# Kernel optimization log

Hardware: AMD Instinct MI355X
Metric: run time of the kernel (lower is better)

The kernel has to match this reference:

```python
import jax, jax.numpy as jnp
import numpy as np
from jax import lax

IMAGE_SIZE = 128
PATCH = 5
STRIDE = 5
ANGLES = np.deg2rad(np.arange(0, 60, 1.0))  # 60 views
N_ANGLES = len(ANGLES)


def _bilinear(img, x, y):
    # img: (H,W); x,y: arbitrary-shape sample coords; zero outside image
    H, W = img.shape
    x0 = jnp.floor(x).astype(jnp.int32)
    y0 = jnp.floor(y).astype(jnp.int32)
    x1, y1 = x0 + 1, y0 + 1
    wx = x - x0.astype(img.dtype)
    wy = y - y0.astype(img.dtype)

    def get(xi, yi):
        valid = (xi >= 0) & (xi < W) & (yi >= 0) & (yi < H)
        v = img[jnp.clip(yi, 0, H - 1), jnp.clip(xi, 0, W - 1)]
        return jnp.where(valid, v, jnp.zeros((), img.dtype))

    return (get(x0, y0) * (1 - wx) * (1 - wy) + get(x1, y0) * wx * (1 - wy)
            + get(x0, y1) * (1 - wx) * wy + get(x1, y1) * wx * wy)


def radon(img, cos_t, sin_t):
    # Discrete Radon forward projection (a=0, no FBP filter): rotate+sum line integrals.
    # img: (H,H) -> sinogram (A, H)
    H = img.shape[0]
    c = (H - 1) / 2.0
    t = jnp.arange(H, dtype=img.dtype) - c  # detector coord
    s = jnp.arange(H, dtype=img.dtype) - c  # along-ray coord
    ct = cos_t[:, None, None]
    st = sin_t[:, None, None]
    x = c + t[None, None, :] * ct - s[None, :, None] * st  # (A,S,T)
    y = c + t[None, None, :] * st + s[None, :, None] * ct
    return _bilinear(img, x, y).sum(axis=1)  # (A,T)


def _patch_starts():
    starts = []
    for i in range(0, IMAGE_SIZE, STRIDE):
        for j in range(0, IMAGE_SIZE, STRIDE):
            if i + PATCH > IMAGE_SIZE or j + PATCH > IMAGE_SIZE:
                continue
            starts.append((i, j))
    return np.array(starts, dtype=np.int32)  # (P,2)


def _build_sinogram_masks(starts):
    c = IMAGE_SIZE // 2
    P = starts.shape[0]
    masks = np.zeros((P, IMAGE_SIZE, IMAGE_SIZE), dtype=np.float32)
    for p, (i, j) in enumerate(starts):
        d0 = np.sqrt((i - c) ** 2 + (j - c) ** 2)
        d1 = np.sqrt((i + PATCH - c) ** 2 + (j + PATCH - c) ** 2)
        if d0 <= c and d1 <= c:
            masks[p, i:i + PATCH, j:j + PATCH] = 1.0
    cos_t = jnp.asarray(np.cos(ANGLES), jnp.float32)
    sin_t = jnp.asarray(np.sin(ANGLES), jnp.float32)
    # sequential map keeps memory bounded while building the 625 base sinograms
    sinos = lax.map(lambda m: radon(m, cos_t, sin_t), jnp.asarray(masks))
    return (sinos > 1e-6).astype(jnp.int32)  # (P, A, H)


def setup_inputs() -> dict:
    key = jax.random.key(0)
    ks = jax.random.split(key, 10)
    starts = _patch_starts()
    sino_masks = _build_sinogram_masks(starts)
    he = lambda k, shp, fan_in: jax.random.normal(k, shp, jnp.float32) * np.sqrt(2.0 / fan_in)
    lin_in = N_ANGLES * IMAGE_SIZE  # 7680
    return {
        "sinogram": jax.random.normal(ks[0], (N_ANGLES, IMAGE_SIZE), jnp.float32),
        "conv1_w": he(ks[1], (32, 1, 3, 3), 9),
        "conv1_b": jnp.zeros((32,), jnp.float32),
        "conv2_w": he(ks[2], (64, 32, 3, 3), 32 * 9),
        "conv2_b": jnp.zeros((64,), jnp.float32),
        "conv3_w": he(ks[3], (1, 64, 3, 3), 64 * 9),
        "conv3_b": jnp.zeros((1,), jnp.float32),
        "lin_w": he(ks[4], (PATCH * PATCH, lin_in), lin_in),
        "lin_b": jnp.zeros((PATCH * PATCH,), jnp.float32),
        "sino_masks": sino_masks,          # (625, 60, 128) int32 0/1
        "starts": jnp.asarray(starts),     # (625, 2) int32
    }


def _conv(x, w, b):
    y = lax.conv_general_dilated(x, w, (1, 1), "SAME",
                                 dimension_numbers=("NCHW", "OIHW", "NCHW"))
    return y + b[None, :, None, None]


def reference(sinogram, conv1_w, conv1_b, conv2_w, conv2_b, conv3_w, conv3_b,
              lin_w, lin_b, sino_masks, starts):
    cos_t = jnp.asarray(np.cos(ANGLES), sinogram.dtype)
    sin_t = jnp.asarray(np.sin(ANGLES), sinogram.dtype)
    # per-patch masked sinograms: (P, 1, A, S)
    masked = (sinogram[None] * sino_masks.astype(sinogram.dtype))[:, None]
    x = jax.nn.relu(_conv(masked, conv1_w, conv1_b))
    x = jax.nn.relu(_conv(x, conv2_w, conv2_b))
    x = _conv(x, conv3_w, conv3_b)
    x = x.reshape(x.shape[0], -1)                       # (P, A*S)
    patches = (x @ lin_w.T + lin_b).reshape(-1, PATCH, PATCH)
    # overlap-average reconstruction (scatter-add + count)
    rows = starts[:, 0][:, None, None] + jnp.arange(PATCH)[None, :, None]
    cols = starts[:, 1][:, None, None] + jnp.arange(PATCH)[None, None, :]
    acc = jnp.zeros((IMAGE_SIZE, IMAGE_SIZE), patches.dtype).at[rows, cols].add(patches)
    cnt = jnp.zeros((IMAGE_SIZE, IMAGE_SIZE), patches.dtype).at[rows, cols].add(1.0)
    recon = jnp.where(cnt > 0, acc / jnp.maximum(cnt, 1.0), 0.0)
    y_hat = jax.nn.sigmoid(recon)
    s_hat = radon(y_hat, cos_t, sin_t)
    return y_hat, s_hat
```

## Files before the change

kernel.cpp:

```cpp
#include <hip/hip_runtime.h>
#include <math.h>

#define A_DIM 60
#define NPATCH 625
#define SENT (1 << 20)

typedef short s16x8 __attribute__((ext_vector_type(8)));
typedef short s16x4 __attribute__((ext_vector_type(4)));
typedef float fx4   __attribute__((ext_vector_type(4)));
typedef float fx2   __attribute__((ext_vector_type(2)));

__device__ __forceinline__ short f2bf(float f) {
    unsigned u = __builtin_bit_cast(unsigned, f);
    unsigned r = (u + 0x7FFFu + ((u >> 16) & 1u)) >> 16;
    return (short)r;
}

__device__ __forceinline__ unsigned cvt_pk_bf16(float lo, float hi) {
    unsigned r;
    asm("v_cvt_pk_bf16_f32 %0, %1, %2" : "=v"(r) : "v"(lo), "v"(hi));
    return r;
}

__device__ __forceinline__ int md5(int x) { return (x >= 5) ? (x - 5) : x; }

__device__ __forceinline__ void wg_barrier() {
    asm volatile("s_waitcnt lgkmcnt(0)" ::: "memory");
    __builtin_amdgcn_s_barrier();
    asm volatile("" ::: "memory");
}

__global__ __launch_bounds__(256) void k_prep(const int* __restrict__ masks,
                                              const float* __restrict__ w1,
                                              const float* __restrict__ w2,
                                              const float* __restrict__ w3,
                                              int* __restrict__ win,
                                              short* __restrict__ w2a,
                                              short* __restrict__ w3a,
                                              float* __restrict__ w1p,
                                              float* __restrict__ patches,
                                              int* __restrict__ actCnt,
                                              int* __restrict__ actList)
{
    const int blk = blockIdx.x, tid = threadIdx.x;
    if (blk < NPATCH) {
        __shared__ int s_f[60][4];
        __shared__ int s_row[64];
        int r = tid >> 2, q = tid & 3;
        if (r < 60) {
            const int4* m4 = (const int4*)(masks + (blk * 60 + r) * 128 + q * 32);
            int first = SENT;
#pragma unroll
            for (int j = 0; j < 8; ++j) {
                int4 v = m4[j];
                int base = q * 32 + j * 4;
                if (v.w) first = min(first, base + 3);
                if (v.z) first = min(first, base + 2);
                if (v.y) first = min(first, base + 1);
                if (v.x) first = min(first, base);
            }
            s_f[r][q] = first;
        }
        __syncthreads();
        if (tid < 60)
            s_row[tid] = min(min(s_f[tid][0], s_f[tid][1]),
                             min(s_f[tid][2], s_f[tid][3]));
        __syncthreads();
        int bact = 0;
        if (tid < 60) {
            int lo = SENT;
            for (int d = -3; d <= 3; ++d) {
                int rr = tid + d;
                if (rr >= 0 && rr < 60) lo = min(lo, s_row[rr]);
            }
            int b;
            if (lo >= SENT) b = SENT;
            else { b = lo - 3; if (b < 0) b = 0; if (b > 96) b = 96; }
            win[blk * 64 + tid] = b;
            bact = (b < 128) ? 1 : 0;
        }
        int cnt = __syncthreads_count(bact);
        if (cnt == 0) {
            if (tid < 50) patches[blk * 50 + tid] = 0.f;
        } else if (tid == 0) {
            int idx = atomicAdd(actCnt, 1);
            actList[idx] = blk;
        }
    } else if (blk < 697) {
        int i = (blk - NPATCH) * 256 + tid;
        int ic = i & 31, ol = (i >> 5) & 15, b2i = i >> 9;
        int ks = b2i % 9, T = b2i / 9;
        int oc = T * 16 + ol, dy = ks / 3, dxx = ks % 3;
        w2a[i] = f2bf(w2[((oc * 32 + ic) * 3 + dy) * 3 + dxx]);
    } else {
#pragma unroll
        for (int jj = 0; jj < 4; ++jj) {
            int i = jj * 256 + tid;
            int k = i & 31, m = (i >> 5) & 15, s = i >> 9;
            int dy = m / 3, dxx = m % 3;
            float v = (m < 9) ? w3[((s * 32 + k) * 3 + dy) * 3 + dxx] : 0.f;
            w3a[i] = f2bf(v);
        }
        if (tid < 144) {
            int j = tid % 9, gp = tid / 9;
            float2 wv;
            wv.x = w1[(2 * gp) * 9 + j];
            wv.y = w1[(2 * gp + 1) * 9 + j];
            ((float2*)w1p)[gp * 9 + j] = wv;
        }
    }
}

__global__ __launch_bounds__(256, 4) void k_pipeline(
    const float* __restrict__ sino,
    const float* __restrict__ w1p, const float* __restrict__ b1,
    const short* __restrict__ w2a, const float* __restrict__ b2w,
    const short* __restrict__ w3a, const float* __restrict__ b3,
    const float* __restrict__ linw,
    const int* __restrict__ masks, const int* __restrict__ win,
    const int* __restrict__ actCnt, const int* __restrict__ actList,
    float* __restrict__ patches)
{
    __shared__ float s_in[5][38];
    __shared__ __align__(16) short s_x1[5][38 * 40];
    __shared__ __align__(16) short s_x2[2][32 * 72];
    __shared__ float s_D[5][9][38];
    __shared__ __align__(16) float s_out3[2][2][32];
    __shared__ float s_lin[200];
    __shared__ int   s_base[64];
    __shared__ __align__(8) int s_db[61][2];

    const int tid = threadIdx.x;

    const int cnt = actCnt[0];
    const int pi  = (int)blockIdx.x >> 1;
    if (pi >= cnt) return;
    const int p    = actList[pi];
    const int half = (int)blockIdx.x & 1;
    const int pbo  = 2 * p + half;

    const int S     = half ? 27 : 0;
    const int in_hi = half ? 59 : 32;
    const int x1lo  = half ? 28 : 0,  x1hi = half ? 59 : 31;
    const int x2lo  = half ? 29 : 0,  x2hi = half ? 59 : 30;
    const int olo   = half ? 30 : 0,  ohi  = half ? 59 : 29;
    const int F     = half ? 23 : 21;

    if (tid < 64)
        s_base[tid] = (tid >= 2 && tid < 62) ? win[p * 64 + (tid - 2)] : SENT;
    if (tid < 30) {
        int sl = tid / 6, c6 = tid % 6;
        s_in[sl][c6 < 3 ? c6 : 32 + c6] = 0.f;
    }
    if (tid < 150) {
        int sl = tid / 30, rem = tid % 30;
        int c6 = rem / 5, q = rem % 5;
        int colz = (c6 < 3) ? c6 : 32 + c6;
        uint4 z; z.x = 0; z.y = 0; z.z = 0; z.w = 0;
        *(uint4*)&s_x1[sl][colz * 40 + q * 8] = z;
    }
    for (int z = tid; z < 270; z += 256) {
        int sl = z / 54, rem = z - sl * 54;
        int mr = rem / 6, c6 = rem - mr * 6;
        s_D[sl][mr][c6 < 3 ? c6 : 32 + c6] = 0.f;
    }

    const int lane   = tid & 63;
    const int n      = lane & 15;
    const int quad   = lane >> 4;
    const int col    = tid & 31;
    const int rowsub = (tid >> 5) & 1;
    const int grp    = __builtin_amdgcn_readfirstlane(tid >> 6);

    s16x8 afrag2[9];
#pragma unroll
    for (int ks = 0; ks < 9; ++ks)
        afrag2[ks] = *(const s16x8*)(w2a + (grp * 9 + ks) * 512 + (n << 5) + (quad << 3));
    const s16x8 w3f0 = *(const s16x8*)(w3a + (n << 5) + (quad << 3));
    const s16x8 w3f1 = *(const s16x8*)(w3a + ((16 + n) << 5) + (quad << 3));
    const float4 bv = *(const float4*)(b2w + (grp << 4) + (quad << 2));
    fx4 binit; binit[0] = bv.x; binit[1] = bv.y; binit[2] = bv.z; binit[3] = bv.w;
    const float b3s = b3[0];

    const int lk = tid >> 3;
    const int lg = tid & 7;
    float lacc = 0.f;
    float pwv[2][4] = {{0.f,0.f,0.f,0.f},{0.f,0.f,0.f,0.f}};
    float pv = 0.f; int pm = 0;
    int m5 = half ? 2 : 0;

    wg_barrier();

    if (tid < 61) {
        int bC = s_base[tid + 2];
        s_db[tid][0] = bC - s_base[tid + 1] - 1;
        s_db[tid][1] = bC - s_base[tid + 3] - 1;
    }

    if (tid < 64) {
        int r = S + (tid >> 5);
        int b = s_base[r + 2];
        if (r <= in_hi && b < 128) {
            int t = b + col;
            pm = masks[(p * A_DIM + r) * 128 + t];
            pv = sino[r * 128 + t];
        }
    }

    for (int f = 0; f < F; ++f) {
        if (tid < 64) {
            int r = S + 2 * f + (tid >> 5);
            int b = s_base[r + 2];
            if (r <= in_hi && b < 128)
                s_in[md5(m5 + (tid >> 5))][col + 3] = pm ? pv : 0.f;
            int r2 = r + 2;
            int b2i = s_base[r2 + 2];
            if (r2 <= in_hi && b2i < 128) {
                int t = b2i + col;
                pm = masks[(p * A_DIM + r2) * 128 + t];
                pv = sino[r2 * 128 + t];
            }
        }
        {
            int q = f - 6;
            if (q >= 0 && tid < 200) {
#pragma unroll
                for (int rs = 0; rs < 2; ++rs) {
                    int r = S + 2 * q + rs;
                    if (r >= olo && r <= ohi) {
                        int b = s_base[r + 2];
                        if (b < 128) {
                            const float4 ov = *(const float4*)
                                &s_out3[(f + 1) & 1][rs][lg * 4];
                            float a = lacc;
                            a = fmaf(ov.x, pwv[rs][0], a);
                            a = fmaf(ov.y, pwv[rs][1], a);
                            a = fmaf(ov.z, pwv[rs][2], a);
                            a = fmaf(ov.w, pwv[rs][3], a);
                            lacc = a;
                        }
                    }
                }
            }
            int q2 = f - 5;
            if (q2 >= 0 && tid < 200) {
#pragma unroll
                for (int rs = 0; rs < 2; ++rs) {
                    int r = S + 2 * q2 + rs;
                    if (r >= olo && r <= ohi) {
                        int b = s_base[r + 2];
                        if (b < 128) {
                            const float* a = linw + lk * (A_DIM * 128)
                                           + r * 128 + b + 4 * lg;
                            pwv[rs][0] = a[0]; pwv[rs][1] = a[1];
                            pwv[rs][2] = a[2]; pwv[rs][3] = a[3];
                        }
                    }
                }
            }
        }
        {
            const int rp = S + 2 * (f - 3);
            const bool act2 = (f >= 3) && (rp <= x2hi) && (rp + 1 >= x2lo);
            if (act2) {
                const int2 ddA = *(const int2*)&s_db[rp][0];
                const int2 ddB = *(const int2*)&s_db[rp + 1][0];
                int dbv[2][2];
                dbv[0][0] = ddA.x; dbv[0][1] = ddB.x;
                dbv[1][0] = ddA.y; dbv[1][1] = ddB.y;
                int slot[4];
                slot[0] = md5(m5 + 3);
                slot[1] = md5(m5 + 4);
                slot[2] = m5;
                slot[3] = md5(m5 + 1);

                fx4 acc[4];
#pragma unroll
                for (int t = 0; t < 4; ++t) acc[t] = binit;

#pragma unroll
                for (int dy = 0; dy < 3; ++dy) {
#pragma unroll
                    for (int t = 0; t < 4; ++t) {
                        int rv = t >> 1;
                        int j;
                        if (dy == 1) {
                            j = ((t & 1) << 4) + n + 2;
                        } else {
                            int idx0 = ((t & 1) << 4) + n
                                     + dbv[dy >> 1][rv];
                            j = min(max(idx0 + 3, 0), 35);
                        }
                        const short* bp = &s_x1[slot[rv + dy]][j * 40 + (quad << 3)];
                        s16x8 bf0 = *(const s16x8*)bp;
                        s16x8 bf1 = *(const s16x8*)(bp + 40);
                        s16x8 bf2 = *(const s16x8*)(bp + 80);
                        acc[t] = __builtin_amdgcn_mfma_f32_16x16x32_bf16(
                                     afrag2[dy * 3 + 0], bf0, acc[t], 0, 0, 0);
                        acc[t] = __builtin_amdgcn_mfma_f32_16x16x32_bf16(
                                     afrag2[dy * 3 + 1], bf1, acc[t], 0, 0, 0);
                        acc[t] = __builtin_amdgcn_mfma_f32_16x16x32_bf16(
                                     afrag2[dy * 3 + 2], bf2, acc[t], 0, 0, 0);
                    }
                }
#pragma unroll
                for (int t = 0; t < 4; ++t) {
                    int rv = t >> 1;
                    int colw = ((t & 1) << 4) + n;
                    unsigned plo = cvt_pk_bf16(fmaxf(acc[t][0], 0.f),
                                               fmaxf(acc[t][1], 0.f));
                    unsigned phi = cvt_pk_bf16(fmaxf(acc[t][2], 0.f),
                                               fmaxf(acc[t][3], 0.f));
                    uint2 pw; pw.x = plo; pw.y = phi;
                    *(uint2*)&s_x2[rv][colw * 72 + (grp << 4) + (quad << 2)] = pw;
                }
            }
        }
        {
            const int rp5 = S + 2 * (f - 5);
            const bool act5 = (f >= 5) && (rp5 <= ohi) && (rp5 + 1 >= olo);
            if (act5 && tid < 64) {
                int rs = tid >> 5, c = tid & 31;
                int r = rp5 + rs;
                if (r >= olo && r <= ohi) {
                    int b = s_base[r + 2];
                    float o = 0.f;
                    if (b < 128) {
                        const int2 dd = *(const int2*)&s_db[r][0];
                        int yb = md5(m5 + 4 + rs);
#pragma unroll
                        for (int dy = 0; dy < 3; ++dy) {
                            int j;
                            if (dy == 0)      j = min(max(c + dd.x + 3, 0), 35);
                            else if (dy == 1) j = c + 2;
                            else              j = min(max(c + dd.y + 3, 0), 35);
                            int ds = md5(yb + dy);
                            const float* Dp = &s_D[ds][dy * 3][0];
                            o += Dp[j] + Dp[38 + j + 1] + Dp[76 + j + 2];
                        }
                    }
                    s_out3[f & 1][rs][c] = o + b3s;
                }
            }
        }
        wg_barrier();

        {
            int r = S + 2 * (f - 1) + rowsub;
            if (f >= 1 && r >= x1lo && r <= x1hi) {
                int b = s_base[r + 2];
                if (b < 128) {
                    int x1b = m5 + rowsub;
                    int sl0 = md5(x1b + 2);
                    int sl1 = md5(x1b + 3);
                    int sl2 = md5(x1b + 4);
                    const int2 dd = *(const int2*)&s_db[r][0];
                    float vin[9];
                    {
                        const float* r0 = &s_in[sl0][0];
                        const float* r1 = &s_in[sl1][0];
                        const float* r2 = &s_in[sl2][0];
                        int j0 = min(max(col + dd.x + 3, 0), 35);
                        int j2 = min(max(col + dd.y + 3, 0), 35);
                        vin[0] = r0[j0]; vin[1] = r0[j0 + 1]; vin[2] = r0[j0 + 2];
                        vin[3] = r1[col + 2]; vin[4] = r1[col + 3]; vin[5] = r1[col + 4];
                        vin[6] = r2[j2]; vin[7] = r2[j2 + 1]; vin[8] = r2[j2 + 2];
                    }
                    const fx2* wpp = (const fx2*)w1p + grp * 36;
                    fx2 ap0 = *(const fx2*)(b1 + grp * 8 + 0);
                    fx2 ap1 = *(const fx2*)(b1 + grp * 8 + 2);
                    fx2 ap2 = *(const fx2*)(b1 + grp * 8 + 4);
                    fx2 ap3 = *(const fx2*)(b1 + grp * 8 + 6);
#pragma unroll
                    for (int j = 0; j < 9; ++j) {
                        fx2 vv; vv[0] = vin[j]; vv[1] = vin[j];
                        ap0 = wpp[j]      * vv + ap0;
                        ap1 = wpp[9 + j]  * vv + ap1;
                        ap2 = wpp[18 + j] * vv + ap2;
                        ap3 = wpp[27 + j] * vv + ap3;
                    }
                    const fx2 z2 = {0.f, 0.f};
                    ap0 = __builtin_elementwise_max(ap0, z2);
                    ap1 = __builtin_elementwise_max(ap1, z2);
                    ap2 = __builtin_elementwise_max(ap2, z2);
                    ap3 = __builtin_elementwise_max(ap3, z2);
                    uint4 pk;
                    pk.x = cvt_pk_bf16(ap0[0], ap0[1]);
                    pk.y = cvt_pk_bf16(ap1[0], ap1[1]);
                    pk.z = cvt_pk_bf16(ap2[0], ap2[1]);
                    pk.w = cvt_pk_bf16(ap3[0], ap3[1]);
                    *(uint4*)&s_x1[sl1][(col + 3) * 40 + grp * 8] = pk;
                }
            }

            const int rp3 = S + 2 * (f - 3);
            const bool act3 = (f >= 3) && (rp3 <= x2hi) && (rp3 + 1 >= x2lo);
            if (act3) {
                int rv = grp & 1, nt = grp >> 1;
                const short* bp = &s_x2[rv][(nt * 16 + n) * 72 + (quad << 3)];
                s16x8 bf0 = *(const s16x8*)bp;
                s16x8 bf1 = *(const s16x8*)(bp + 32);
                fx4 a3 = {0.f, 0.f, 0.f, 0.f};
                a3 = __builtin_amdgcn_mfma_f32_16x16x32_bf16(w3f0, bf0, a3, 0, 0, 0);
                a3 = __builtin_amdgcn_mfma_f32_16x16x32_bf16(w3f1, bf1, a3, 0, 0, 0);
                int dslot = md5(m5 + 4 + rv);
#pragma unroll
                for (int e = 0; e < 4; ++e) {
                    int m = (quad << 2) + e;
                    if (m < 9) s_D[dslot][m][3 + nt * 16 + n] = a3[e];
                }
            }
        }
        wg_barrier();
        m5 = md5(m5 + 2);
    }

    if (tid < 200) s_lin[tid] = lacc;
    __syncthreads();
    if (tid < 25) {
        float s = 0.f;
#pragma unroll
        for (int g = 0; g < 8; ++g) s += s_lin[tid * 8 + g];
        patches[pbo * 25 + tid] = s;
    }
}

__global__ __launch_bounds__(256) void k_img(const float* __restrict__ patches,
                                             const float* __restrict__ linb,
                                             float* __restrict__ out)
{
    const int blk = blockIdx.x, tid = threadIdx.x;
    if (blk < 64) {
        int i = blk * 256 + tid;
        int y = i >> 7, x = i & 127;
        float rec = 0.f;
        if (y < 125 && x < 125) {
            int pp = (y / 5) * 25 + (x / 5);
            int k  = (y % 5) * 5 + (x % 5);
            rec = patches[(2 * pp) * 25 + k] + patches[(2 * pp + 1) * 25 + k]
                + linb[k];
        }
        out[i] = 1.f / (1.f + expf(-rec));
    } else {
        int j = (blk - 64) * 256 + tid;
        if (j < A_DIM * 128) out[128 * 128 + j] = 0.f;
    }
}

__global__ __launch_bounds__(256) void k_rad(const float* __restrict__ yimg,
                                             float* __restrict__ out)
{
    __shared__ float img[128 * 128];
    __shared__ float s_r[2][128];
    const int tid = threadIdx.x;
    const int a   = blockIdx.x >> 2;
    const int cch = blockIdx.x & 3;

#pragma unroll
    for (int j = 0; j < 16; ++j) {
        int idx = j * 256 + tid;
        ((float4*)img)[idx] = ((const float4*)yimg)[idx];
    }
    __syncthreads();

    const int t  = tid & 127;
    const int ss = tid >> 7;
    double ang = (double)a * (M_PI / 180.0);
    float ct = (float)cos(ang);
    float st = (float)sin(ang);
    const float c = 63.5f;
    float tt = (float)t - c;
    float sum = 0.f;
    int s0 = cch * 32 + ss * 16;
    for (int s = s0; s < s0 + 16; ++s) {
        float sv = (float)s - c;
        float x = c + tt * ct - sv * st;
        float y = c + tt * st + sv * ct;
        float fx = floorf(x), fy = floorf(y);
        int x0 = (int)fx, y0 = (int)fy;
        float wx = x - fx, wy = y - fy;
        bool vx0 = (x0 >= 0) & (x0 < 128), vx1 = (x0 + 1 >= 0) & (x0 + 1 < 128);
        bool vy0 = (y0 >= 0) & (y0 < 128), vy1 = (y0 + 1 >= 0) & (y0 + 1 < 128);
        int xc0 = min(max(x0, 0), 127), xc1 = min(max(x0 + 1, 0), 127);
        int yc0 = min(max(y0, 0), 127), yc1 = min(max(y0 + 1, 0), 127);
        float v00 = (vx0 & vy0) ? img[yc0 * 128 + xc0] : 0.f;
        float v10 = (vx1 & vy0) ? img[yc0 * 128 + xc1] : 0.f;
        float v01 = (vx0 & vy1) ? img[yc1 * 128 + xc0] : 0.f;
        float v11 = (vx1 & vy1) ? img[yc1 * 128 + xc1] : 0.f;
        sum += v00 * (1.f - wx) * (1.f - wy)
             + v10 * wx * (1.f - wy)
             + v01 * (1.f - wx) * wy
             + v11 * wx * wy;
    }
    s_r[ss][t] = sum;
    __syncthreads();
    if (ss == 0)
        atomicAdd(out + 128 * 128 + a * 128 + t, s_r[0][t] + s_r[1][t]);
}

extern "C" void kernel_launch(void* const* d_in, const int* in_sizes, int n_in,
                              void* d_out, int out_size, void* d_ws, size_t ws_size,
                              hipStream_t stream)
{
    (void)in_sizes; (void)n_in; (void)out_size; (void)ws_size;

    const float* sino  = (const float*)d_in[0];
    const float* w1    = (const float*)d_in[1];
    const float* b1    = (const float*)d_in[2];
    const float* w2    = (const float*)d_in[3];
    const float* b2    = (const float*)d_in[4];
    const float* w3    = (const float*)d_in[5];
    const float* b3    = (const float*)d_in[6];
    const float* lw    = (const float*)d_in[7];
    const float* lb    = (const float*)d_in[8];
    const int*   masks = (const int*)d_in[9];

    float* out = (float*)d_out;

    char* ws = (char*)d_ws;
    float* patches = (float*)ws;
    int*   win     = (int*)(ws + 128 * 1024);
    short* w2a     = (short*)(ws + 288 * 1024);
    short* w3a     = (short*)(ws + 328 * 1024);
    int*   actCnt  = (int*)(ws + 332 * 1024);
    int*   actList = (int*)(ws + 332 * 1024 + 64);
    float* w1p     = (float*)(ws + 336 * 1024);

    hipMemsetAsync(actCnt, 0, sizeof(int), stream);
    k_prep<<<698, 256, 0, stream>>>(masks, w1, w2, w3, win, w2a, w3a, w1p,
                                    patches, actCnt, actList);
    k_pipeline<<<2 * NPATCH, 256, 0, stream>>>(sino, w1p, b1, w2a, b2, w3a, b3,
                                               lw, masks, win, actCnt, actList,
                                               patches);
    k_img<<<94, 256, 0, stream>>>(patches, lb, out);
    k_rad<<<4 * A_DIM, 256, 0, stream>>>(out, out);
}
```

Measured before the change: 173.0 us.

## Repartition conv2 MFMA work by output row and channel-half per wave

```diff
diff --git a/kernel.cpp b/kernel.cpp
--- a/kernel.cpp
+++ b/kernel.cpp
@@ -111,7 +111,7 @@
     }
 }
 
-__global__ __launch_bounds__(256, 4) void k_pipeline(
+__global__ __launch_bounds__(256) void k_pipeline(
     const float* __restrict__ sino,
     const float* __restrict__ w1p, const float* __restrict__ b1,
     const short* __restrict__ w2a, const float* __restrict__ b2w,
@@ -171,15 +171,18 @@
     const int col    = tid & 31;
     const int rowsub = (tid >> 5) & 1;
     const int grp    = __builtin_amdgcn_readfirstlane(tid >> 6);
-
-    s16x8 afrag2[9];
+    const int rvw    = grp & 1;
+    const int ohw    = grp >> 1;
+
+    s16x8 afrag2[9][2];
 #pragma unroll
     for (int ks = 0; ks < 9; ++ks)
-        afrag2[ks] = *(const s16x8*)(w2a + (grp * 9 + ks) * 512 + (n << 5) + (quad << 3));
+#pragma unroll
+        for (int ocb = 0; ocb < 2; ++ocb)
+            afrag2[ks][ocb] = *(const s16x8*)(w2a
+                + ((((ohw * 2 + ocb) * 9 + ks)) << 9) + (n << 5) + (quad << 3));
     const s16x8 w3f0 = *(const s16x8*)(w3a + (n << 5) + (quad << 3));
     const s16x8 w3f1 = *(const s16x8*)(w3a + ((16 + n) << 5) + (quad << 3));
-    const float4 bv = *(const float4*)(b2w + (grp << 4) + (quad << 2));
-    fx4 binit; binit[0] = bv.x; binit[1] = bv.y; binit[2] = bv.z; binit[3] = bv.w;
     const float b3s = b3[0];
 
     const int lk = tid >> 3;
@@ -263,56 +266,56 @@
             const int rp = S + 2 * (f - 3);
             const bool act2 = (f >= 3) && (rp <= x2hi) && (rp + 1 >= x2lo);
             if (act2) {
-                const int2 ddA = *(const int2*)&s_db[rp][0];
-                const int2 ddB = *(const int2*)&s_db[rp + 1][0];
-                int dbv[2][2];
-                dbv[0][0] = ddA.x; dbv[0][1] = ddB.x;
-                dbv[1][0] = ddA.y; dbv[1][1] = ddB.y;
-                int slot[4];
-                slot[0] = md5(m5 + 3);
-                slot[1] = md5(m5 + 4);
-                slot[2] = m5;
-                slot[3] = md5(m5 + 1);
+                const int rw = rp + rvw;
+                const int2 dd = *(const int2*)&s_db[rw][0];
+                const int slotA = md5(m5 + 3 + rvw);
+                const int slotB = md5(m5 + 4 + rvw);
+                const int slotC = md5(m5 + rvw);
 
                 fx4 acc[4];
 #pragma unroll
-                for (int t = 0; t < 4; ++t) acc[t] = binit;
+                for (int t = 0; t < 4; ++t) {
+                    acc[t][0] = 0.f; acc[t][1] = 0.f;
+                    acc[t][2] = 0.f; acc[t][3] = 0.f;
+                }
 
 #pragma unroll
                 for (int dy = 0; dy < 3; ++dy) {
-#pragma unroll
-                    for (int t = 0; t < 4; ++t) {
-                        int rv = t >> 1;
+                    const int slot = (dy == 0) ? slotA : (dy == 1 ? slotB : slotC);
+                    const int d    = (dy == 0) ? dd.x : (dy == 1 ? -1 : dd.y);
+#pragma unroll
+                    for (int th = 0; th < 2; ++th) {
                         int j;
-                        if (dy == 1) {
-                            j = ((t & 1) << 4) + n + 2;
-                        } else {
-                            int idx0 = ((t & 1) << 4) + n
-                                     + dbv[dy >> 1][rv];
-                            j = min(max(idx0 + 3, 0), 35);
-                        }
-                        const short* bp = &s_x1[slot[rv + dy]][j * 40 + (quad << 3)];
+                        if (dy == 1) j = (th << 4) + n + 2;
+                        else         j = min(max((th << 4) + n + d + 3, 0), 35);
+                        const short* bp = &s_x1[slot][j * 40 + (quad << 3)];
                         s16x8 bf0 = *(const s16x8*)bp;
                         s16x8 bf1 = *(const s16x8*)(bp + 40);
                         s16x8 bf2 = *(const s16x8*)(bp + 80);
-                        acc[t] = __builtin_amdgcn_mfma_f32_16x16x32_bf16(
-                                     afrag2[dy * 3 + 0], bf0, acc[t], 0, 0, 0);
-                        acc[t] = __builtin_amdgcn_mfma_f32_16x16x32_bf16(
-                                     afrag2[dy * 3 + 1], bf1, acc[t], 0, 0, 0);
-                        acc[t] = __builtin_amdgcn_mfma_f32_16x16x32_bf16(
-                                     afrag2[dy * 3 + 2], bf2, acc[t], 0, 0, 0);
+#pragma unroll
+                        for (int ocb = 0; ocb < 2; ++ocb) {
+                            int t = (ocb << 1) | th;
+                            acc[t] = __builtin_amdgcn_mfma_f32_16x16x32_bf16(
+                                         afrag2[dy * 3 + 0][ocb], bf0, acc[t], 0, 0, 0);
+                            acc[t] = __builtin_amdgcn_mfma_f32_16x16x32_bf16(
+                                         afrag2[dy * 3 + 1][ocb], bf1, acc[t], 0, 0, 0);
+                            acc[t] = __builtin_amdgcn_mfma_f32_16x16x32_bf16(
+                                         afrag2[dy * 3 + 2][ocb], bf2, acc[t], 0, 0, 0);
+                        }
                     }
                 }
 #pragma unroll
                 for (int t = 0; t < 4; ++t) {
-                    int rv = t >> 1;
-                    int colw = ((t & 1) << 4) + n;
-                    unsigned plo = cvt_pk_bf16(fmaxf(acc[t][0], 0.f),
-                                               fmaxf(acc[t][1], 0.f));
-                    unsigned phi = cvt_pk_bf16(fmaxf(acc[t][2], 0.f),
-                                               fmaxf(acc[t][3], 0.f));
+                    int ocb = t >> 1, th = t & 1;
+                    int obi = (ohw << 1) | ocb;
+                    const float4 bb = *(const float4*)(b2w + (obi << 4) + (quad << 2));
+                    unsigned plo = cvt_pk_bf16(fmaxf(acc[t][0] + bb.x, 0.f),
+                                               fmaxf(acc[t][1] + bb.y, 0.f));
+                    unsigned phi = cvt_pk_bf16(fmaxf(acc[t][2] + bb.z, 0.f),
+                                               fmaxf(acc[t][3] + bb.w, 0.f));
                     uint2 pw; pw.x = plo; pw.y = phi;
-                    *(uint2*)&s_x2[rv][colw * 72 + (grp << 4) + (quad << 2)] = pw;
+                    int colw = (th << 4) + n;
+                    *(uint2*)&s_x2[rvw][colw * 72 + (obi << 4) + (quad << 2)] = pw;
                 }
             }
         }
```

New measurement: 193.6 us. 11.9% more time.
